# Optimization experiments

Measured on AMD Instinct MI355X. Metric: run time of the kernel, lower is better.

The kernel has to match this reference:

```python
import jax, jax.numpy as jnp
import numpy as np

B, N, C, H = 4, 2048, 512, 8
DH = C // H
HID = 4 * C
EPS = 1e-5

def _ln(x, w, b):
    mu = jnp.mean(x, axis=-1, keepdims=True)
    var = jnp.mean(jnp.square(x - mu), axis=-1, keepdims=True)
    return (x - mu) * jax.lax.rsqrt(var + EPS) * w + b

def setup_inputs() -> dict:
    key = jax.random.key(0)
    ks = jax.random.split(key, 8)
    s = 0.02
    return {
        "x": jax.random.normal(ks[0], (B, N, C), jnp.float32),
        "qkv_w": jax.random.normal(ks[1], (3 * C, C), jnp.float32) * s,
        "proj_w": jax.random.normal(ks[2], (C, C), jnp.float32) * s,
        "proj_b": jnp.zeros((C,), jnp.float32),
        "rpb_table": jax.random.normal(ks[3], (2 * N - 1, H), jnp.float32) * s,
        "n1_w": jnp.ones((C,), jnp.float32),
        "n1_b": jnp.zeros((C,), jnp.float32),
        "n2_w": jnp.ones((C,), jnp.float32),
        "n2_b": jnp.zeros((C,), jnp.float32),
        "fc1_w": jax.random.normal(ks[4], (HID, C), jnp.float32) * s,
        "fc1_b": jnp.zeros((HID,), jnp.float32),
        "fc2_w": jax.random.normal(ks[5], (C, HID), jnp.float32) * s,
        "fc2_b": jnp.zeros((C,), jnp.float32),
    }

def reference(x, qkv_w, proj_w, proj_b, rpb_table, n1_w, n1_b, n2_w, n2_b,
              fc1_w, fc1_b, fc2_w, fc2_b):
    # ---- attention branch (pre-norm) ----
    h = _ln(x, n1_w, n1_b)
    qkv = h @ qkv_w.T                                   # [B,N,3C]
    qkv = qkv.reshape(B, N, 3, H, DH)
    q = jnp.transpose(qkv[:, :, 0], (0, 2, 1, 3))       # [B,H,N,DH]
    k = jnp.transpose(qkv[:, :, 1], (0, 2, 1, 3))
    v = jnp.transpose(qkv[:, :, 2], (0, 2, 1, 3))
    scale = DH ** -0.5
    attn = jnp.einsum('bhqd,bhkd->bhqk', q, k) * scale  # [B,H,N,N]
    # learnable relative position bias
    coords = jnp.arange(N)
    rel_idx = coords[None, :] - coords[:, None] + (N - 1)  # [N,N]
    bias = rpb_table[rel_idx]                            # [N,N,H]
    attn = attn + jnp.transpose(bias, (2, 0, 1))[None]
    attn = jax.nn.softmax(attn, axis=-1)
    out = jnp.einsum('bhqk,bhkd->bhqd', attn, v)         # [B,H,N,DH]
    out = jnp.transpose(out, (0, 2, 1, 3)).reshape(B, N, C)
    x = x + out @ proj_w.T + proj_b
    # ---- MLP branch (pre-norm) ----
    h2 = _ln(x, n2_w, n2_b)
    h2 = jax.nn.gelu(h2 @ fc1_w.T + fc1_b, approximate=False)
    x = x + h2 @ fc2_w.T + fc2_b
    return x
```

## Files before the change

kernel.cpp:

```cpp
#include <hip/hip_runtime.h>
#include <hip/hip_bf16.h>
#include <math.h>

typedef __bf16 bf16x8 __attribute__((ext_vector_type(8)));
typedef float  f32x4  __attribute__((ext_vector_type(4)));
typedef short  s16x8  __attribute__((ext_vector_type(8)));
typedef unsigned int u32x2 __attribute__((ext_vector_type(2)));
typedef unsigned int u32x4 __attribute__((ext_vector_type(4)));

#define B_   4
#define N_   2048
#define C_   512
#define H_   8
#define DH_  64
#define HID_ 2048
#define MTOK 8192
#define LOG2E 1.4426950408889634f
#define QSCALE 0.18033688011112042f

__device__ inline void gld_lds16(const void* g, void* l) {
  __builtin_amdgcn_global_load_lds((const __attribute__((address_space(1))) void*)g,
                                   (__attribute__((address_space(3))) void*)l,
                                   16, 0, 0);
}

__device__ inline unsigned pack2_bf16(float a, float b) {
  unsigned pa = __builtin_bit_cast(unsigned, a) + 0x8000u;
  unsigned pb = __builtin_bit_cast(unsigned, b) + 0x8000u;
  return __builtin_amdgcn_perm(pb, pa, 0x07060302u);
}

__device__ inline unsigned cvtpk2(float a, float b) {
  unsigned r;
  asm("v_cvt_pk_bf16_f32 %0, %1, %2" : "=v"(r) : "v"(a), "v"(b));
  return r;
}

template<int EPI>
__device__ inline void epi_store(float v, int row, int col, int N,
    const float* __restrict__ bias, const float* __restrict__ resid,
    float* __restrict__ fout, __bf16* __restrict__ bout,
    __bf16* __restrict__ qo, __bf16* __restrict__ ko, __bf16* __restrict__ vo)
{
  if (EPI == 0) {
    const int b = row >> 11, n = row & (N_ - 1);
    const int s = col >> 9, h = (col >> 6) & (H_ - 1), d = col & (DH_ - 1);
    if (s == 2) {
      vo[((((size_t)b * H_ + h) * DH_ + d) << 11) + n] = (__bf16)v;
    } else if (s == 1) {
      ko[((((size_t)b * H_ + h) * N_ + n) << 6) + d] = (__bf16)v;
    } else {
      qo[((((size_t)b * H_ + h) * N_ + n) << 6) + d] = (__bf16)(v * QSCALE);
    }
  } else if (EPI == 1) {
    const size_t idx = (size_t)row * N + col;
    fout[idx] = v + bias[col] + resid[idx];
  } else {
    const float xg = v + bias[col];
    const float x2 = xg * xg;
    const float u  = __builtin_fmaf(0.044715f * x2, xg, xg);
    const float t  = __builtin_amdgcn_exp2f(u * 2.3022082f);
    const float g  = xg * t * __builtin_amdgcn_rcpf(t + 1.0f);
    bout[(size_t)row * N + col] = (__bf16)g;
  }
}

template<int EPI, int BN>
__global__ __launch_bounds__(512, 4) void gemm512(
    const __bf16* __restrict__ A, const __bf16* __restrict__ Bw,
    int M, int N, int K,
    const float* __restrict__ bias, const float* __restrict__ resid,
    float* __restrict__ fout, __bf16* __restrict__ bout,
    __bf16* __restrict__ qo, __bf16* __restrict__ ko, __bf16* __restrict__ vo)
{
  constexpr int NT = (BN == 128) ? 4 : 2;
  __shared__ __align__(16) __bf16 a_lds[2][128 * 32];
  __shared__ __align__(16) __bf16 b_lds[2][BN * 32];
  const int tid  = threadIdx.x;
  const int wave = tid >> 6, lane = tid & 63;
  const int quad = lane >> 4, l16 = lane & 15;
  const int bm = blockIdx.x * 128, bn = blockIdx.y * BN;
  const int wr = (wave >> 1) * 32;
  const int wc = (wave & 1) * (BN == 128 ? 64 : 32);
  const int srow = tid >> 2;
  const int c4   = lane & 3;

  const f32x4 fzero = {0.f, 0.f, 0.f, 0.f};
  f32x4 acc[2][NT];
  #pragma unroll
  for (int i = 0; i < 2; ++i)
    #pragma unroll
    for (int j = 0; j < NT; ++j) acc[i][j] = fzero;

  auto stage = [&](int buf, int k0) {
    gld_lds16(A + (size_t)(bm + srow) * K + k0 + c4 * 8, &a_lds[buf][wave * 512]);
    if (BN == 128 || wave < 4)
      gld_lds16(Bw + (size_t)(bn + srow) * K + k0 + c4 * 8, &b_lds[buf][wave * 512]);
  };

  const int nk = K >> 5;
  stage(0, 0);
  for (int ki = 0; ki < nk; ++ki) {
    const int cur = ki & 1;
    __syncthreads();
    if (ki + 1 < nk) stage(cur ^ 1, (ki + 1) << 5);
    bf16x8 af[2], bf[NT];
    #pragma unroll
    for (int t = 0; t < 2; ++t)
      af[t] = *(const bf16x8*)&a_lds[cur][(wr + t * 16 + l16) * 32 + quad * 8];
    #pragma unroll
    for (int t = 0; t < NT; ++t)
      bf[t] = *(const bf16x8*)&b_lds[cur][(wc + t * 16 + l16) * 32 + quad * 8];
    #pragma unroll
    for (int mt = 0; mt < 2; ++mt)
      #pragma unroll
      for (int nt = 0; nt < NT; ++nt)
        acc[mt][nt] = __builtin_amdgcn_mfma_f32_16x16x32_bf16(af[mt], bf[nt], acc[mt][nt], 0, 0, 0);
  }

  #pragma unroll
  for (int mt = 0; mt < 2; ++mt)
    #pragma unroll
    for (int nt = 0; nt < NT; ++nt)
      #pragma unroll
      for (int r = 0; r < 4; ++r)
        epi_store<EPI>(acc[mt][nt][r], bm + wr + mt * 16 + quad * 4 + r,
                       bn + wc + nt * 16 + l16, N,
                       bias, resid, fout, bout, qo, ko, vo);
}

template<int EPI>
__global__ __launch_bounds__(256, 3) void gemm256(
    const __bf16* __restrict__ A, const __bf16* __restrict__ Bw,
    int M, int N, int K,
    const float* __restrict__ bias, const float* __restrict__ resid,
    float* __restrict__ fout, __bf16* __restrict__ bout,
    __bf16* __restrict__ qo, __bf16* __restrict__ ko, __bf16* __restrict__ vo)
{
  __shared__ __align__(16) __bf16 a_lds[2][128 * 32];
  __shared__ __align__(16) __bf16 b_lds[2][128 * 32];
  const int tid  = threadIdx.x;
  const int wave = tid >> 6, lane = tid & 63;
  const int quad = lane >> 4, l16 = lane & 15;
  const int bm = blockIdx.x * 128, bn = blockIdx.y * 128;
  const int wr = (wave >> 1) * 64;
  const int wc = (wave & 1) * 64;
  const int srow = tid >> 2;
  const int c4   = lane & 3;

  const f32x4 fzero = {0.f, 0.f, 0.f, 0.f};
  f32x4 acc[4][4];
  #pragma unroll
  for (int i = 0; i < 4; ++i)
    #pragma unroll
    for (int j = 0; j < 4; ++j) acc[i][j] = fzero;

  auto stage = [&](int buf, int k0) {
    gld_lds16(A + (size_t)(bm + srow) * K + k0 + c4 * 8, &a_lds[buf][wave * 512]);
    gld_lds16(A + (size_t)(bm + 64 + srow) * K + k0 + c4 * 8, &a_lds[buf][2048 + wave * 512]);
    gld_lds16(Bw + (size_t)(bn + srow) * K + k0 + c4 * 8, &b_lds[buf][wave * 512]);
    gld_lds16(Bw + (size_t)(bn + 64 + srow) * K + k0 + c4 * 8, &b_lds[buf][2048 + wave * 512]);
  };

  const int nk = K >> 5;
  stage(0, 0);
  for (int ki = 0; ki < nk; ++ki) {
    const int cur = ki & 1;
    __syncthreads();
    if (ki + 1 < nk) stage(cur ^ 1, (ki + 1) << 5);
    bf16x8 af[4], bf[4];
    #pragma unroll
    for (int t = 0; t < 4; ++t)
      af[t] = *(const bf16x8*)&a_lds[cur][(wr + t * 16 + l16) * 32 + quad * 8];
    #pragma unroll
    for (int t = 0; t < 4; ++t)
      bf[t] = *(const bf16x8*)&b_lds[cur][(wc + t * 16 + l16) * 32 + quad * 8];
    #pragma unroll
    for (int mt = 0; mt < 4; ++mt)
      #pragma unroll
      for (int nt = 0; nt < 4; ++nt)
        acc[mt][nt] = __builtin_amdgcn_mfma_f32_16x16x32_bf16(af[mt], bf[nt], acc[mt][nt], 0, 0, 0);
  }

  if (EPI == 0 && bn >= 1024) {
    const int b = bm >> 11;
    #pragma unroll
    for (int mt = 0; mt < 4; ++mt) {
      const int n = (bm + wr + mt * 16 + quad * 4) & (N_ - 1);
      #pragma unroll
      for (int nt = 0; nt < 4; ++nt) {
        const int col = bn + wc + nt * 16 + l16;
        const int h = (col >> 6) & (H_ - 1), d = col & (DH_ - 1);
        u32x2 pkd;
        pkd.x = cvtpk2(acc[mt][nt][0], acc[mt][nt][1]);
        pkd.y = cvtpk2(acc[mt][nt][2], acc[mt][nt][3]);
        *(u32x2*)(vo + ((((size_t)b * H_ + h) * DH_ + d) << 11) + n) = pkd;
      }
    }
  } else {
    #pragma unroll
    for (int mt = 0; mt < 4; ++mt)
      #pragma unroll
      for (int nt = 0; nt < 4; ++nt)
        #pragma unroll
        for (int r = 0; r < 4; ++r)
          epi_store<EPI>(acc[mt][nt][r], bm + wr + mt * 16 + quad * 4 + r,
                         bn + wc + nt * 16 + l16, N,
                         bias, resid, fout, bout, qo, ko, vo);
  }
}

__device__ inline void ln_row(const float* __restrict__ xr,
                              const float* __restrict__ w, const float* __restrict__ b,
                              __bf16* __restrict__ orow, int lane)
{
  float4 v0 = ((const float4*)xr)[lane];
  float4 v1 = ((const float4*)xr)[lane + 64];
  float s = v0.x + v0.y + v0.z + v0.w + v1.x + v1.y + v1.z + v1.w;
  float q = v0.x*v0.x + v0.y*v0.y + v0.z*v0.z + v0.w*v0.w
          + v1.x*v1.x + v1.y*v1.y + v1.z*v1.z + v1.w*v1.w;
  #pragma unroll
  for (int off = 32; off >= 1; off >>= 1) {
    s += __shfl_xor(s, off, 64);
    q += __shfl_xor(q, off, 64);
  }
  const float mu  = s * (1.0f / C_);
  const float var = q * (1.0f / C_) - mu * mu;
  const float rs  = rsqrtf(var + 1e-5f);
  float4 w0 = ((const float4*)w)[lane], w1 = ((const float4*)w)[lane + 64];
  float4 b0 = ((const float4*)b)[lane], b1 = ((const float4*)b)[lane + 64];
  const int c0 = lane * 4;
  orow[c0 + 0]       = (__bf16)((v0.x - mu) * rs * w0.x + b0.x);
  orow[c0 + 1]       = (__bf16)((v0.y - mu) * rs * w0.y + b0.y);
  orow[c0 + 2]       = (__bf16)((v0.z - mu) * rs * w0.z + b0.z);
  orow[c0 + 3]       = (__bf16)((v0.w - mu) * rs * w0.w + b0.w);
  orow[256 + c0 + 0] = (__bf16)((v1.x - mu) * rs * w1.x + b1.x);
  orow[256 + c0 + 1] = (__bf16)((v1.y - mu) * rs * w1.y + b1.y);
  orow[256 + c0 + 2] = (__bf16)((v1.z - mu) * rs * w1.z + b1.z);
  orow[256 + c0 + 3] = (__bf16)((v1.w - mu) * rs * w1.w + b1.w);
}

__global__ __launch_bounds__(256) void ln_kernel(
    const float* __restrict__ x, const float* __restrict__ w,
    const float* __restrict__ b, __bf16* __restrict__ out)
{
  const int wave = threadIdx.x >> 6, lane = threadIdx.x & 63;
  const int tok  = blockIdx.x * 4 + wave;
  ln_row(x + (size_t)tok * C_, w, b, out + (size_t)tok * C_, lane);
}

__global__ __launch_bounds__(256) void castln_kernel(
    const float* __restrict__ s0, const float* __restrict__ s1,
    const float* __restrict__ s2, const float* __restrict__ s3,
    __bf16* __restrict__ d0, __bf16* __restrict__ d1,
    __bf16* __restrict__ d2, __bf16* __restrict__ d3,
    const float* __restrict__ x, const float* __restrict__ n1w,
    const float* __restrict__ n1b, __bf16* __restrict__ hbuf)
{
  if (blockIdx.x < 3072) {
    const int i = (blockIdx.x * 256 + threadIdx.x) * 4;
    const float* s; __bf16* d; int off;
    if (i < 786432)       { s = s0; d = d0; off = i; }
    else if (i < 1048576) { s = s1; d = d1; off = i - 786432; }
    else if (i < 2097152) { s = s2; d = d2; off = i - 1048576; }
    else                  { s = s3; d = d3; off = i - 2097152; }
    const float4 v = *(const float4*)(s + off);
    u32x2 pk;
    pk.x = pack2_bf16(v.x, v.y);
    pk.y = pack2_bf16(v.z, v.w);
    *(u32x2*)(d + off) = pk;
  } else {
    const int wave = threadIdx.x >> 6, lane = threadIdx.x & 63;
    const int tok  = (blockIdx.x - 3072) * 4 + wave;
    ln_row(x + (size_t)tok * C_, n1w, n1b, hbuf + (size_t)tok * C_, lane);
  }
}

__global__ __launch_bounds__(256, 2) void flash_kernel(
    const __bf16* __restrict__ qb, const __bf16* __restrict__ kb,
    const __bf16* __restrict__ vtg, const float* __restrict__ rpb,
    __bf16* __restrict__ outb, int bh0)
{
  __shared__ __align__(16) __bf16 kbufs[2][8192];
  __shared__ __align__(16) __bf16 vbufs[2][8192];
  __shared__ __align__(16) float  biasF[2192];
  const int tid  = threadIdx.x;
  const int wave = tid >> 6, lane = tid & 63;
  const int quad = lane >> 4, l16 = lane & 15;
  const int bh = blockIdx.y + bh0, h = bh & (H_ - 1);
  const int q0 = blockIdx.x * 128;
  const int boff = 1920 - q0;

  for (int i = tid; i < 2192; i += 256) {
    int ridx = i + boff;
    ridx = ridx < 0 ? 0 : (ridx > 2 * N_ - 2 ? 2 * N_ - 2 : ridx);
    biasF[i] = rpb[(size_t)ridx * H_ + h] * LOG2E;
  }

  const __bf16* qptr = qb  + (size_t)bh * N_ * DH_;
  const __bf16* kptr = kb  + (size_t)bh * N_ * DH_;
  const __bf16* vtp  = vtg + (size_t)bh * N_ * DH_;

  bf16x8 qf[2][2];
  #pragma unroll
  for (int mt = 0; mt < 2; ++mt)
    #pragma unroll
    for (int ks = 0; ks < 2; ++ks)
      qf[mt][ks] = *(const bf16x8*)(qptr +
          (size_t)(q0 + wave * 32 + mt * 16 + l16) * DH_ + ks * 32 + quad * 8);

  const f32x4 fzero = {0.f, 0.f, 0.f, 0.f};
  f32x4 o[2][4];
  f32x4 la[2] = {fzero, fzero};
  #pragma unroll
  for (int mt = 0; mt < 2; ++mt)
    #pragma unroll
    for (int dt = 0; dt < 4; ++dt) o[mt][dt] = fzero;

  const s16x8 ones_s = {(short)0x3F80, (short)0x3F80, (short)0x3F80, (short)0x3F80,
                        (short)0x3F80, (short)0x3F80, (short)0x3F80, (short)0x3F80};
  const bf16x8 ones8 = __builtin_bit_cast(bf16x8, ones_s);

  const int slr = lane >> 2;
  const int slc = lane & 3;
  const int vswz = (slr & 3) ^ ((slr >> 2) & 3);
  const int rswz = (l16 & 3) ^ ((l16 >> 2) & 3);

  auto stageK = [&](int buf, int kcn) {
    #pragma unroll
    for (int j = 0; j < 4; ++j) {
      const int idx = wave * 4 + j;
      const int ks = idx & 1, g = idx >> 1;
      const int R = g * 16 + slr;
      const int m = R & 31;
      const int pr = (R & ~31) | (((m >> 2) & 3) << 3) | (((m >> 4) & 1) << 2) | (m & 3);
      gld_lds16(kptr + (size_t)(kcn + pr) * DH_ + ks * 32 + slc * 8,
                &kbufs[buf][ks * 4096 + g * 512]);
    }
  };
  auto stageV = [&](int buf, int kcn) {
    #pragma unroll
    for (int j = 0; j < 4; ++j) {
      const int idx = wave * 4 + j;
      const int ks2 = idx & 3, gg = idx >> 2;
      gld_lds16(vtp + (size_t)(gg * 16 + slr) * N_ + kcn + ks2 * 32 + (slc ^ vswz) * 8,
                &vbufs[buf][ks2 * 2048 + gg * 512]);
    }
  };

  const int bb0 = 127 + quad * 8 - wave * 32 - l16;

  stageK(0, 0);
  stageV(0, 0);
  for (int it = 0; it < 16; ++it) {
    const int cur = it & 1;
    const int kc = it << 7;
    __syncthreads();
    if (it < 15) {
      stageK(cur ^ 1, kc + 128);
      stageV(cur ^ 1, kc + 128);
    }

    bf16x8 vv[16];
    #pragma unroll
    for (int c = 0; c < 4; ++c)
      #pragma unroll
      for (int dt = 0; dt < 4; ++dt)
        vv[c * 4 + dt] = *(const bf16x8*)&vbufs[cur][c * 2048 + l16 * 32 +
                                                     (quad ^ rswz) * 8 + dt * 512];

    unsigned pk[2][8][2];
    const float* bp = biasF + kc + bb0;
    #pragma unroll
    for (int ct = 0; ct < 8; ++ct) {
      const int co = (ct >> 1) * 32 + (ct & 1) * 4;
      const bf16x8 kf0 = *(const bf16x8*)&kbufs[cur][(ct * 16 + l16) * 32 + quad * 8];
      const bf16x8 kf1 = *(const bf16x8*)&kbufs[cur][4096 + (ct * 16 + l16) * 32 + quad * 8];
      const f32x4 c0 = {bp[co], bp[co + 1], bp[co + 2], bp[co + 3]};
      const f32x4 c1 = {bp[co - 16], bp[co - 15], bp[co - 14], bp[co - 13]};
      f32x4 s0 = __builtin_amdgcn_mfma_f32_16x16x32_bf16(kf0, qf[0][0], c0, 0, 0, 0);
      s0 = __builtin_amdgcn_mfma_f32_16x16x32_bf16(kf1, qf[0][1], s0, 0, 0, 0);
      f32x4 s1 = __builtin_amdgcn_mfma_f32_16x16x32_bf16(kf0, qf[1][0], c1, 0, 0, 0);
      s1 = __builtin_amdgcn_mfma_f32_16x16x32_bf16(kf1, qf[1][1], s1, 0, 0, 0);
      {
        const float p0 = __builtin_amdgcn_exp2f(s0[0]);
        const float p1 = __builtin_amdgcn_exp2f(s0[1]);
        const float p2 = __builtin_amdgcn_exp2f(s0[2]);
        const float p3 = __builtin_amdgcn_exp2f(s0[3]);
        pk[0][ct][0] = cvtpk2(p0, p1);
        pk[0][ct][1] = cvtpk2(p2, p3);
      }
      {
        const float p0 = __builtin_amdgcn_exp2f(s1[0]);
        const float p1 = __builtin_amdgcn_exp2f(s1[1]);
        const float p2 = __builtin_amdgcn_exp2f(s1[2]);
        const float p3 = __builtin_amdgcn_exp2f(s1[3]);
        pk[1][ct][0] = cvtpk2(p0, p1);
        pk[1][ct][1] = cvtpk2(p2, p3);
      }
    }

    #pragma unroll
    for (int c = 0; c < 4; ++c) {
      const u32x4 t0 = {pk[0][2*c][0], pk[0][2*c][1], pk[0][2*c+1][0], pk[0][2*c+1][1]};
      const u32x4 t1 = {pk[1][2*c][0], pk[1][2*c][1], pk[1][2*c+1][0], pk[1][2*c+1][1]};
      const bf16x8 pf0 = __builtin_bit_cast(bf16x8, t0);
      const bf16x8 pf1 = __builtin_bit_cast(bf16x8, t1);
      la[0] = __builtin_amdgcn_mfma_f32_16x16x32_bf16(ones8, pf0, la[0], 0, 0, 0);
      la[1] = __builtin_amdgcn_mfma_f32_16x16x32_bf16(ones8, pf1, la[1], 0, 0, 0);
      #pragma unroll
      for (int dt = 0; dt < 4; ++dt) {
        const bf16x8 vf = vv[c * 4 + dt];
        o[0][dt] = __builtin_amdgcn_mfma_f32_16x16x32_bf16(vf, pf0, o[0][dt], 0, 0, 0);
        o[1][dt] = __builtin_amdgcn_mfma_f32_16x16x32_bf16(vf, pf1, o[1][dt], 0, 0, 0);
      }
    }
  }

  const int b = bh >> 3;
  #pragma unroll
  for (int mt = 0; mt < 2; ++mt) {
    const float inv = 1.0f / la[mt][0];
    const int qg = q0 + wave * 32 + mt * 16 + l16;
    __bf16* orow = outb + ((size_t)(b * N_ + qg)) * C_ + h * DH_ + quad * 4;
    #pragma unroll
    for (int dt = 0; dt < 4; ++dt) {
      u32x2 pkd;
      pkd.x = cvtpk2(o[mt][dt][0] * inv, o[mt][dt][1] * inv);
      pkd.y = cvtpk2(o[mt][dt][2] * inv, o[mt][dt][3] * inv);
      *(u32x2*)(orow + dt * 16) = pkd;
    }
  }
}

extern "C" void kernel_launch(void* const* d_in, const int* in_sizes, int n_in,
                              void* d_out, int out_size, void* d_ws, size_t ws_size,
                              hipStream_t stream)
{
  const float* x      = (const float*)d_in[0];
  const float* qkv_w  = (const float*)d_in[1];
  const float* proj_w = (const float*)d_in[2];
  const float* proj_b = (const float*)d_in[3];
  const float* rpb    = (const float*)d_in[4];
  const float* n1w    = (const float*)d_in[5];
  const float* n1b    = (const float*)d_in[6];
  const float* n2w    = (const float*)d_in[7];
  const float* n2b    = (const float*)d_in[8];
  const float* fc1_w  = (const float*)d_in[9];
  const float* fc1_b  = (const float*)d_in[10];
  const float* fc2_w  = (const float*)d_in[11];
  const float* fc2_b  = (const float*)d_in[12];

  char* ws = (char*)d_ws;
  __bf16* hbuf = (__bf16*)(ws + 0);
  __bf16* qbuf = (__bf16*)(ws + 8388608);
  __bf16* kbuf = (__bf16*)(ws + 16777216);
  __bf16* vbuf = (__bf16*)(ws + 25165824);
  __bf16* gelu = (__bf16*)(ws + 0);
  __bf16* wq   = (__bf16*)(ws + 33554432);
  __bf16* wp   = (__bf16*)(ws + 35127296);
  __bf16* w1   = (__bf16*)(ws + 35651584);
  __bf16* w2   = (__bf16*)(ws + 37748736);
  __bf16* attn = (__bf16*)(ws + 39845888);
  __bf16* h2in = attn;
  float*  x1   = (float*)(ws + 48234496);
  float*  outp = (float*)d_out;

  castln_kernel<<<5120, 256, 0, stream>>>(qkv_w, proj_w, fc1_w, fc2_w,
      wq, wp, w1, w2, x, n1w, n1b, hbuf);

  gemm256<0><<<dim3(64, 12), 256, 0, stream>>>(hbuf, wq, MTOK, 1536, 512,
      nullptr, nullptr, nullptr, nullptr, qbuf, kbuf, vbuf);

  flash_kernel<<<dim3(16, 32), 256, 0, stream>>>(qbuf, kbuf, vbuf, rpb, attn, 0);

  gemm512<1, 64><<<dim3(64, 8), 512, 0, stream>>>(attn, wp, MTOK, 512, 512,
      proj_b, x, x1, nullptr, nullptr, nullptr, nullptr);

  ln_kernel<<<2048, 256, 0, stream>>>(x1, n2w, n2b, h2in);

  gemm256<2><<<dim3(64, 16), 256, 0, stream>>>(h2in, w1, MTOK, 2048, 512,
      fc1_b, nullptr, nullptr, gelu, nullptr, nullptr, nullptr);

  gemm512<1, 64><<<dim3(64, 8), 512, 0, stream>>>(gelu, w2, MTOK, 512, 2048,
      fc2_b, x1, outp, nullptr, nullptr, nullptr, nullptr);
}
```

Before: 240.0 us.

## Triple-buffer GEMM LDS staging with explicit vmcnt waits and raw barriers

Both GEMM kernels move from double to triple LDS buffering, keeping two K-slices of global-to-LDS loads in flight. __syncthreads is replaced by s_waitcnt vmcnt with a count matching the outstanding loads, plus s_barrier, so a wave waits only for the oldest stage. The aim is to hide more global load latency behind MFMA work. The cost is 50% more LDS per block, which may lower occupancy under the launch bounds. Correctness also depends on the hand-set vmcnt counts and on the LDS reads of a buffer finishing before it is overwritten.

```diff
diff --git a/kernel.cpp b/kernel.cpp
--- a/kernel.cpp
+++ b/kernel.cpp
@@ -74,8 +74,8 @@
     __bf16* __restrict__ qo, __bf16* __restrict__ ko, __bf16* __restrict__ vo)
 {
   constexpr int NT = (BN == 128) ? 4 : 2;
-  __shared__ __align__(16) __bf16 a_lds[2][128 * 32];
-  __shared__ __align__(16) __bf16 b_lds[2][BN * 32];
+  __shared__ __align__(16) __bf16 a_lds[3][128 * 32];
+  __shared__ __align__(16) __bf16 b_lds[3][BN * 32];
   const int tid  = threadIdx.x;
   const int wave = tid >> 6, lane = tid & 63;
   const int quad = lane >> 4, l16 = lane & 15;
@@ -84,6 +84,7 @@
   const int wc = (wave & 1) * (BN == 128 ? 64 : 32);
   const int srow = tid >> 2;
   const int c4   = lane & 3;
+  const bool hasB = (BN == 128) || (wave < 4);
 
   const f32x4 fzero = {0.f, 0.f, 0.f, 0.f};
   f32x4 acc[2][NT];
@@ -94,16 +95,27 @@
 
   auto stage = [&](int buf, int k0) {
     gld_lds16(A + (size_t)(bm + srow) * K + k0 + c4 * 8, &a_lds[buf][wave * 512]);
-    if (BN == 128 || wave < 4)
+    if (hasB)
       gld_lds16(Bw + (size_t)(bn + srow) * K + k0 + c4 * 8, &b_lds[buf][wave * 512]);
   };
 
   const int nk = K >> 5;
   stage(0, 0);
+  stage(1, 32);
+  int cur = 0;
   for (int ki = 0; ki < nk; ++ki) {
-    const int cur = ki & 1;
-    __syncthreads();
-    if (ki + 1 < nk) stage(cur ^ 1, (ki + 1) << 5);
+    if (ki + 1 < nk) {
+      if (hasB) asm volatile("s_waitcnt vmcnt(2)" ::: "memory");
+      else      asm volatile("s_waitcnt vmcnt(1)" ::: "memory");
+    } else {
+      asm volatile("s_waitcnt vmcnt(0)" ::: "memory");
+    }
+    __builtin_amdgcn_s_barrier();
+    __builtin_amdgcn_sched_barrier(0);
+    if (ki + 2 < nk) {
+      int nb = cur + 2; if (nb >= 3) nb -= 3;
+      stage(nb, (ki + 2) << 5);
+    }
     bf16x8 af[2], bf[NT];
     #pragma unroll
     for (int t = 0; t < 2; ++t)
@@ -116,6 +128,7 @@
       #pragma unroll
       for (int nt = 0; nt < NT; ++nt)
         acc[mt][nt] = __builtin_amdgcn_mfma_f32_16x16x32_bf16(af[mt], bf[nt], acc[mt][nt], 0, 0, 0);
+    ++cur; if (cur == 3) cur = 0;
   }
 
   #pragma unroll
@@ -137,8 +150,8 @@
     float* __restrict__ fout, __bf16* __restrict__ bout,
     __bf16* __restrict__ qo, __bf16* __restrict__ ko, __bf16* __restrict__ vo)
 {
-  __shared__ __align__(16) __bf16 a_lds[2][128 * 32];
-  __shared__ __align__(16) __bf16 b_lds[2][128 * 32];
+  __shared__ __align__(16) __bf16 a_lds[3][128 * 32];
+  __shared__ __align__(16) __bf16 b_lds[3][128 * 32];
   const int tid  = threadIdx.x;
   const int wave = tid >> 6, lane = tid & 63;
   const int quad = lane >> 4, l16 = lane & 15;
@@ -164,10 +177,17 @@
 
   const int nk = K >> 5;
   stage(0, 0);
+  stage(1, 32);
+  int cur = 0;
   for (int ki = 0; ki < nk; ++ki) {
-    const int cur = ki & 1;
-    __syncthreads();
-    if (ki + 1 < nk) stage(cur ^ 1, (ki + 1) << 5);
+    if (ki + 1 < nk) asm volatile("s_waitcnt vmcnt(4)" ::: "memory");
+    else             asm volatile("s_waitcnt vmcnt(0)" ::: "memory");
+    __builtin_amdgcn_s_barrier();
+    __builtin_amdgcn_sched_barrier(0);
+    if (ki + 2 < nk) {
+      int nb = cur + 2; if (nb >= 3) nb -= 3;
+      stage(nb, (ki + 2) << 5);
+    }
     bf16x8 af[4], bf[4];
     #pragma unroll
     for (int t = 0; t < 4; ++t)
@@ -180,6 +200,7 @@
       #pragma unroll
       for (int nt = 0; nt < 4; ++nt)
         acc[mt][nt] = __builtin_amdgcn_mfma_f32_16x16x32_bf16(af[mt], bf[nt], acc[mt][nt], 0, 0, 0);
+    ++cur; if (cur == 3) cur = 0;
   }
 
   if (EPI == 0 && bn >= 1024) {
```

Measured after the change: 247.6 us. 3.2% more time.

## Overlap weight casts with flash attention and vectorize Q/K epilogue stores

Applied to the files above, without the earlier changes.

Only the qkv weight is now cast to bf16 in the first kernel. The proj, fc1 and fc2 weight casts move into the flash attention kernel and run right after the first K/V tile loads are issued, so that memory-bound work hides behind attention. The QKV GEMM's Q/K tiles swap the MFMA operand order, which gives each lane 4 contiguous head-dim values, so it can store packed 8-byte bf16 vectors instead of scalar scattered stores. In exchange the flash kernel carries extra global traffic and registers, which could slow its main loop.

```diff
diff --git a/kernel.cpp b/kernel.cpp
--- a/kernel.cpp
+++ b/kernel.cpp
@@ -39,20 +39,9 @@
 template<int EPI>
 __device__ inline void epi_store(float v, int row, int col, int N,
     const float* __restrict__ bias, const float* __restrict__ resid,
-    float* __restrict__ fout, __bf16* __restrict__ bout,
-    __bf16* __restrict__ qo, __bf16* __restrict__ ko, __bf16* __restrict__ vo)
-{
-  if (EPI == 0) {
-    const int b = row >> 11, n = row & (N_ - 1);
-    const int s = col >> 9, h = (col >> 6) & (H_ - 1), d = col & (DH_ - 1);
-    if (s == 2) {
-      vo[((((size_t)b * H_ + h) * DH_ + d) << 11) + n] = (__bf16)v;
-    } else if (s == 1) {
-      ko[((((size_t)b * H_ + h) * N_ + n) << 6) + d] = (__bf16)v;
-    } else {
-      qo[((((size_t)b * H_ + h) * N_ + n) << 6) + d] = (__bf16)(v * QSCALE);
-    }
-  } else if (EPI == 1) {
+    float* __restrict__ fout, __bf16* __restrict__ bout)
+{
+  if (EPI == 1) {
     const size_t idx = (size_t)row * N + col;
     fout[idx] = v + bias[col] + resid[idx];
   } else {
@@ -70,8 +59,7 @@
     const __bf16* __restrict__ A, const __bf16* __restrict__ Bw,
     int M, int N, int K,
     const float* __restrict__ bias, const float* __restrict__ resid,
-    float* __restrict__ fout, __bf16* __restrict__ bout,
-    __bf16* __restrict__ qo, __bf16* __restrict__ ko, __bf16* __restrict__ vo)
+    float* __restrict__ fout, __bf16* __restrict__ bout)
 {
   constexpr int NT = (BN == 128) ? 4 : 2;
   __shared__ __align__(16) __bf16 a_lds[2][128 * 32];
@@ -125,8 +113,7 @@
       #pragma unroll
       for (int r = 0; r < 4; ++r)
         epi_store<EPI>(acc[mt][nt][r], bm + wr + mt * 16 + quad * 4 + r,
-                       bn + wc + nt * 16 + l16, N,
-                       bias, resid, fout, bout, qo, ko, vo);
+                       bn + wc + nt * 16 + l16, N, bias, resid, fout, bout);
 }
 
 template<int EPI>
@@ -147,6 +134,7 @@
   const int wc = (wave & 1) * 64;
   const int srow = tid >> 2;
   const int c4   = lane & 3;
+  const bool swapqk = (EPI == 0) && (bn < 1024);
 
   const f32x4 fzero = {0.f, 0.f, 0.f, 0.f};
   f32x4 acc[4][4];
@@ -175,26 +163,53 @@
     #pragma unroll
     for (int t = 0; t < 4; ++t)
       bf[t] = *(const bf16x8*)&b_lds[cur][(wc + t * 16 + l16) * 32 + quad * 8];
-    #pragma unroll
-    for (int mt = 0; mt < 4; ++mt)
-      #pragma unroll
-      for (int nt = 0; nt < 4; ++nt)
-        acc[mt][nt] = __builtin_amdgcn_mfma_f32_16x16x32_bf16(af[mt], bf[nt], acc[mt][nt], 0, 0, 0);
-  }
-
-  if (EPI == 0 && bn >= 1024) {
+    if (swapqk) {
+      #pragma unroll
+      for (int mt = 0; mt < 4; ++mt)
+        #pragma unroll
+        for (int nt = 0; nt < 4; ++nt)
+          acc[mt][nt] = __builtin_amdgcn_mfma_f32_16x16x32_bf16(bf[nt], af[mt], acc[mt][nt], 0, 0, 0);
+    } else {
+      #pragma unroll
+      for (int mt = 0; mt < 4; ++mt)
+        #pragma unroll
+        for (int nt = 0; nt < 4; ++nt)
+          acc[mt][nt] = __builtin_amdgcn_mfma_f32_16x16x32_bf16(af[mt], bf[nt], acc[mt][nt], 0, 0, 0);
+    }
+  }
+
+  if (EPI == 0) {
     const int b = bm >> 11;
-    #pragma unroll
-    for (int mt = 0; mt < 4; ++mt) {
-      const int n = (bm + wr + mt * 16 + quad * 4) & (N_ - 1);
-      #pragma unroll
-      for (int nt = 0; nt < 4; ++nt) {
-        const int col = bn + wc + nt * 16 + l16;
-        const int h = (col >> 6) & (H_ - 1), d = col & (DH_ - 1);
-        u32x2 pkd;
-        pkd.x = cvtpk2(acc[mt][nt][0], acc[mt][nt][1]);
-        pkd.y = cvtpk2(acc[mt][nt][2], acc[mt][nt][3]);
-        *(u32x2*)(vo + ((((size_t)b * H_ + h) * DH_ + d) << 11) + n) = pkd;
+    if (bn >= 1024) {
+      #pragma unroll
+      for (int mt = 0; mt < 4; ++mt) {
+        const int n = (bm + wr + mt * 16 + quad * 4) & (N_ - 1);
+        #pragma unroll
+        for (int nt = 0; nt < 4; ++nt) {
+          const int col = bn + wc + nt * 16 + l16;
+          const int h = (col >> 6) & (H_ - 1), d = col & (DH_ - 1);
+          u32x2 pkd;
+          pkd.x = cvtpk2(acc[mt][nt][0], acc[mt][nt][1]);
+          pkd.y = cvtpk2(acc[mt][nt][2], acc[mt][nt][3]);
+          *(u32x2*)(vo + ((((size_t)b * H_ + h) * DH_ + d) << 11) + n) = pkd;
+        }
+      }
+    } else {
+      const int sqk = bn >> 9;
+      __bf16* dst = sqk ? ko : qo;
+      const float sc = sqk ? 1.0f : QSCALE;
+      #pragma unroll
+      for (int mt = 0; mt < 4; ++mt) {
+        const int n = (bm + wr + mt * 16 + l16) & (N_ - 1);
+        #pragma unroll
+        for (int nt = 0; nt < 4; ++nt) {
+          const int w = bn + wc + nt * 16 + quad * 4;
+          const int h = (w >> 6) & (H_ - 1), d = w & (DH_ - 1);
+          u32x2 pkd;
+          pkd.x = cvtpk2(acc[mt][nt][0] * sc, acc[mt][nt][1] * sc);
+          pkd.y = cvtpk2(acc[mt][nt][2] * sc, acc[mt][nt][3] * sc);
+          *(u32x2*)(dst + ((((size_t)b * H_ + h) * N_ + n) << 6) + d) = pkd;
+        }
       }
     }
   } else {
@@ -205,8 +220,7 @@
         #pragma unroll
         for (int r = 0; r < 4; ++r)
           epi_store<EPI>(acc[mt][nt][r], bm + wr + mt * 16 + quad * 4 + r,
-                         bn + wc + nt * 16 + l16, N,
-                         bias, resid, fout, bout, qo, ko, vo);
+                         bn + wc + nt * 16 + l16, N, bias, resid, fout, bout);
   }
 }
 
@@ -250,28 +264,20 @@
 }
 
 __global__ __launch_bounds__(256) void castln_kernel(
-    const float* __restrict__ s0, const float* __restrict__ s1,
-    const float* __restrict__ s2, const float* __restrict__ s3,
-    __bf16* __restrict__ d0, __bf16* __restrict__ d1,
-    __bf16* __restrict__ d2, __bf16* __restrict__ d3,
+    const float* __restrict__ s0, __bf16* __restrict__ d0,
     const float* __restrict__ x, const float* __restrict__ n1w,
     const float* __restrict__ n1b, __bf16* __restrict__ hbuf)
 {
-  if (blockIdx.x < 3072) {
+  if (blockIdx.x < 768) {
     const int i = (blockIdx.x * 256 + threadIdx.x) * 4;
-    const float* s; __bf16* d; int off;
-    if (i < 786432)       { s = s0; d = d0; off = i; }
-    else if (i < 1048576) { s = s1; d = d1; off = i - 786432; }
-    else if (i < 2097152) { s = s2; d = d2; off = i - 1048576; }
-    else                  { s = s3; d = d3; off = i - 2097152; }
-    const float4 v = *(const float4*)(s + off);
+    const float4 v = *(const float4*)(s0 + i);
     u32x2 pk;
     pk.x = pack2_bf16(v.x, v.y);
     pk.y = pack2_bf16(v.z, v.w);
-    *(u32x2*)(d + off) = pk;
+    *(u32x2*)(d0 + i) = pk;
   } else {
     const int wave = threadIdx.x >> 6, lane = threadIdx.x & 63;
-    const int tok  = (blockIdx.x - 3072) * 4 + wave;
+    const int tok  = (blockIdx.x - 768) * 4 + wave;
     ln_row(x + (size_t)tok * C_, n1w, n1b, hbuf + (size_t)tok * C_, lane);
   }
 }
@@ -279,7 +285,10 @@
 __global__ __launch_bounds__(256, 2) void flash_kernel(
     const __bf16* __restrict__ qb, const __bf16* __restrict__ kb,
     const __bf16* __restrict__ vtg, const float* __restrict__ rpb,
-    __bf16* __restrict__ outb, int bh0)
+    __bf16* __restrict__ outb, int bh0,
+    const float* __restrict__ cpw, const float* __restrict__ cf1,
+    const float* __restrict__ cf2, __bf16* __restrict__ cwp,
+    __bf16* __restrict__ cw1, __bf16* __restrict__ cw2)
 {
   __shared__ __align__(16) __bf16 kbufs[2][8192];
   __shared__ __align__(16) __bf16 vbufs[2][8192];
@@ -352,6 +361,24 @@
 
   stageK(0, 0);
   stageV(0, 0);
+
+  {
+    const int gid = (blockIdx.y * 16 + blockIdx.x) * 256 + tid;
+    #pragma unroll 1
+    for (int j = gid; j < 589824; j += 131072) {
+      const int i = j * 4;
+      const float* s; __bf16* d; int off;
+      if (i < 262144)       { s = cpw; d = cwp; off = i; }
+      else if (i < 1310720) { s = cf1; d = cw1; off = i - 262144; }
+      else                  { s = cf2; d = cw2; off = i - 1310720; }
+      const float4 v = *(const float4*)(s + off);
+      u32x2 pk;
+      pk.x = pack2_bf16(v.x, v.y);
+      pk.y = pack2_bf16(v.z, v.w);
+      *(u32x2*)(d + off) = pk;
+    }
+  }
+
   for (int it = 0; it < 16; ++it) {
     const int cur = it & 1;
     const int kc = it << 7;
@@ -466,16 +493,16 @@
   float*  x1   = (float*)(ws + 48234496);
   float*  outp = (float*)d_out;
 
-  castln_kernel<<<5120, 256, 0, stream>>>(qkv_w, proj_w, fc1_w, fc2_w,
-      wq, wp, w1, w2, x, n1w, n1b, hbuf);
+  castln_kernel<<<2816, 256, 0, stream>>>(qkv_w, wq, x, n1w, n1b, hbuf);
 
   gemm256<0><<<dim3(64, 12), 256, 0, stream>>>(hbuf, wq, MTOK, 1536, 512,
       nullptr, nullptr, nullptr, nullptr, qbuf, kbuf, vbuf);
 
-  flash_kernel<<<dim3(16, 32), 256, 0, stream>>>(qbuf, kbuf, vbuf, rpb, attn, 0);
+  flash_kernel<<<dim3(16, 32), 256, 0, stream>>>(qbuf, kbuf, vbuf, rpb, attn, 0,
+      proj_w, fc1_w, fc2_w, wp, w1, w2);
 
   gemm512<1, 64><<<dim3(64, 8), 512, 0, stream>>>(attn, wp, MTOK, 512, 512,
-      proj_b, x, x1, nullptr, nullptr, nullptr, nullptr);
+      proj_b, x, x1, nullptr);
 
   ln_kernel<<<2048, 256, 0, stream>>>(x1, n2w, n2b, h2in);
 
@@ -483,5 +510,5 @@
       fc1_b, nullptr, nullptr, gelu, nullptr, nullptr, nullptr);
 
   gemm512<1, 64><<<dim3(64, 8), 512, 0, stream>>>(gelu, w2, MTOK, 512, 2048,
-      fc2_b, x1, outp, nullptr, nullptr, nullptr, nullptr);
-}
+      fc2_b, x1, outp, nullptr);
+}
```

Result: slower. 250.4 us (+4.3%).
